# Optimization experiments

Hardware: AMD Instinct MI355X
Metric: run time of the kernel (lower is better)

Reference implementation:

```python
import jax, jax.numpy as jnp
import numpy as np
from jax import lax

EPS = 0.1        # entropic regularization
MAX_ITER = 100   # Sinkhorn iteration budget
THRESH = 0.1     # early-stop threshold on err = mean_b sum_i |u - u_prev|
B, N, D = 16, 1024, 64


def setup_inputs() -> dict:
    key = jax.random.key(0)
    k1, k2 = jax.random.split(key)
    x = jax.random.normal(k1, (B, N, D), dtype=jnp.float32)
    y = jax.random.normal(k2, (B, N, D), dtype=jnp.float32)
    return {"x": x, "y": y}


def _lse(A):
    # Faithful to the original (unstabilized) lse: log(sum(exp(A)) + 1e-6)
    return jnp.log(jnp.exp(A).sum(-1) + 1e-6)


def _M(C, u, v):
    # (-C_ij + u_i + v_j) / eps
    return (-C + u[..., :, None] + v[..., None, :]) / EPS


def _cost_matrix(x, y):
    # (avoids materializing the [B, N, N, D] difference tensor; same math for p=2)
    x2 = (x * x).sum(-1)                         # [B, N]
    y2 = (y * y).sum(-1)                         # [B, N]
    xy = jnp.einsum('bid,bjd->bij', x, y)        # [B, N, N]
    return x2[..., :, None] + y2[..., None, :] - 2.0 * xy


def reference(x, y):
    x = jax.nn.softmax(x, axis=-1)
    y = jax.nn.softmax(y, axis=-1)
    C = _cost_matrix(x, y)                       # [B, N, N]
    n = x.shape[-2]
    log_mu = jnp.log(1.0 / n + 1e-8)             # mu = nu = uniform 1/n (scalar broadcast)
    u0 = jnp.zeros((x.shape[0], n), dtype=C.dtype)
    v0 = jnp.zeros_like(u0)

    def cond(carry):
        _, _, i, err = carry
        return jnp.logical_and(i < MAX_ITER, err >= THRESH)

    def body(carry):
        u, v, i, _ = carry
        u1 = u
        u = EPS * (log_mu - _lse(_M(C, u, v))) + u
        v = EPS * (log_mu - _lse(jnp.swapaxes(_M(C, u, v), -2, -1))) + v
        err = jnp.abs(u - u1).sum(-1).mean()
        return (u, v, i + 1, err)

    u, v, _, _ = lax.while_loop(
        cond, body, (u0, v0, jnp.int32(0), jnp.float32(jnp.inf)))

    pi = jnp.exp(_M(C, u, v))                    # transport plan [B, N, N]
    cost = (pi * C).sum((-2, -1))                # [B]
    return cost.mean()                           # reduction='mean'
```

## Files before the change

### kernel.cpp

```cpp
#include <hip/hip_runtime.h>
#include <hip/hip_bf16.h>
#include <math.h>

#define BATCH 16
#define NPTS 1024
#define DIM 64
#define EPSF 0.1f
#define INV_EPS 10.0f
#define MAX_ITER 100
#define THRESHF 0.1f
#define LSTRIDE 72

typedef _Float16 h8 __attribute__((ext_vector_type(8)));
typedef short short8v __attribute__((ext_vector_type(8)));
typedef float float4v __attribute__((ext_vector_type(4)));

#define ATOMIC_ST(p, v) \
  __hip_atomic_store((p), (v), __ATOMIC_RELAXED, __HIP_MEMORY_SCOPE_AGENT)
#define ATOMIC_LD(p) \
  __hip_atomic_load((p), __ATOMIC_RELAXED, __HIP_MEMORY_SCOPE_AGENT)

__device__ inline float waveSum(float x) {
#pragma unroll
  for (int off = 32; off; off >>= 1) x += __shfl_xor(x, off, 64);
  return x;
}
__device__ inline float waveMax(float x) {
#pragma unroll
  for (int off = 32; off; off >>= 1) x = fmaxf(x, __shfl_xor(x, off, 64));
  return x;
}
__device__ inline long long packTag(int tag, float v) {
  return ((long long)tag << 32) | (long long)__float_as_uint(v);
}
__device__ inline long long pollTag(long long* p, int tag) {
  long long w;
  do { w = ATOMIC_LD(p); } while ((int)(w >> 32) < tag);
  return w;
}

__global__ __launch_bounds__(512, 2) void sinkhorn_fused(
    const float* __restrict__ x, const float* __restrict__ y,
    __hip_bfloat16* __restrict__ syh,
    float* __restrict__ y2,
    long long* __restrict__ partialT,
    long long* __restrict__ csT,
    long long* __restrict__ deltaT,
    long long* __restrict__ flags,
    float* __restrict__ errB,
    float* __restrict__ costPart,
    float* __restrict__ out) {
  __shared__ __attribute__((aligned(16))) short xs[64 * LSTRIDE];
  __shared__ __attribute__((aligned(16))) short ys[2][64 * LSTRIDE];
  __shared__ __attribute__((aligned(16))) short os[2][64 * LSTRIDE];
  __shared__ __attribute__((aligned(16))) float wLDS[NPTS];
  __shared__ __attribute__((aligned(16))) float colpart[8][NPTS];
  __shared__ __attribute__((aligned(16))) float red[16][66];
  __shared__ float x2L[64];
  __shared__ float derr[8];
  __shared__ float errbL[BATCH];
  const int t = threadIdx.x;
  const int blk = blockIdx.x;
  const int wave = t >> 6, lane = t & 63;
  const int batch = (blk & 7) + 8 * (blk >> 7);
  const int kslot = (blk >> 3) & 15;
  const float log_mu = logf(1.0f / 1024.0f + 1e-8f);
  const float mu_c = 1.0f / 1024.0f + 1e-8f;

#pragma unroll
  for (int rr = 0; rr < 8; rr++) {
    int rl = wave * 8 + rr;
    int gr = batch * NPTS + kslot * 64 + rl;
    float xv = x[(size_t)gr * DIM + lane];
    float mx = waveMax(xv);
    float ex = __expf(xv - mx);
    float sx = waveSum(ex);
    float px = ex / sx;
    __hip_bfloat16 hbx = (__hip_bfloat16)px;
    xs[rl * LSTRIDE + lane] = *(const short*)&hbx;
    float sqx = waveSum(px * px);
    if (lane == 0) x2L[rl] = sqx;
    float yv = y[(size_t)gr * DIM + lane];
    float my = waveMax(yv);
    float ey = __expf(yv - my);
    float sy = waveSum(ey);
    float py = ey / sy;
    __hip_bfloat16 hby = (__hip_bfloat16)py;
    unsigned bits = *(const unsigned short*)&hby;
    unsigned nb = __shfl_down(bits, 1);
    if ((lane & 1) == 0)
      ATOMIC_ST((unsigned*)((unsigned short*)syh + (size_t)gr * DIM + lane),
                bits | (nb << 16));
    float sqy = waveSum(py * py);
    if (lane == 0) ATOMIC_ST(&y2[gr], sqy);
  }
  __syncthreads();
  if (t == 0) ATOMIC_ST(&flags[batch * 16 + kslot], (long long)1 << 32);
  if (t < 16) {
    while ((int)(ATOMIC_LD(&flags[batch * 16 + t]) >> 32) < 1) {}
  }
  __syncthreads();

  const int m = lane & 15, q = lane >> 4;
  const int g = lane >> 3, sub = lane & 7;
  const int sw = wave & 3, ts = wave >> 2;
  short8v a0 = *(const short8v*)&xs[(sw * 16 + m) * LSTRIDE + q * 8];
  short8v a1 = *(const short8v*)&xs[(sw * 16 + m) * LSTRIDE + 32 + q * 8];
  float xa[4];
#pragma unroll
  for (int reg = 0; reg < 4; reg++) xa[reg] = x2L[sw * 16 + q * 4 + reg];
  float kaf[8][16];
#pragma unroll
  for (int k = 0; k < 8; k++) {
    {
      int idx = t;
#pragma unroll
      for (int rep = 0; rep < 2; rep++, idx += 512) {
        int r = idx >> 3, c = idx & 7;
        *(short8v*)&ys[r >> 6][(r & 63) * LSTRIDE + c * 8] = *(const short8v*)(
            (const short*)syh + ((size_t)batch * NPTS + 128 * k + r) * DIM + c * 8);
      }
    }
    __syncthreads();
    const int jt = 2 * k + ts;
    float4v accv[4];
#pragma unroll
    for (int tj = 0; tj < 4; tj++) {
      short8v b0 = *(const short8v*)&ys[ts][(tj * 16 + m) * LSTRIDE + q * 8];
      short8v b1 = *(const short8v*)&ys[ts][(tj * 16 + m) * LSTRIDE + 32 + q * 8];
      float4v c = {0.f, 0.f, 0.f, 0.f};
      c = __builtin_amdgcn_mfma_f32_16x16x32_bf16(a0, b0, c, 0, 0, 0);
      c = __builtin_amdgcn_mfma_f32_16x16x32_bf16(a1, b1, c, 0, 0, 0);
      accv[tj] = c;
    }
#pragma unroll
    for (int tj = 0; tj < 4; tj++) {
      float y2v = y2[(size_t)batch * NPTS + jt * 64 + tj * 16 + m];
#pragma unroll
      for (int reg = 0; reg < 4; reg++) {
        float C = xa[reg] + y2v - 2.0f * accv[tj][reg];
        _Float16 kv = (_Float16)__expf(-INV_EPS * C);
        os[ts][(sw * 16 + q * 4 + reg) * LSTRIDE + tj * 16 + m] = *(const short*)&kv;
      }
    }
    __syncthreads();
    {
      int e0 = (2 * k) & 7, e1 = (2 * k + 1) & 7;
      if (g == e0 || g == e1) {
        const short* srcp = (g == e0) ? &os[0][0] : &os[1][0];
#pragma unroll
        for (int rr = 0; rr < 8; rr++) {
          h8 v = *(const h8*)&srcp[(wave * 8 + rr) * LSTRIDE + sub * 8];
#pragma unroll
          for (int n = 0; n < 8; n++) {
            if (k < 4) kaf[rr][n] = (float)v[n];
            else kaf[rr][8 + n] = (float)v[n];
          }
        }
      }
    }
    __syncthreads();
  }

  for (int j = t; j < NPTS; j += 512) wLDS[j] = 1.f;
  __syncthreads();

  float eu[8], euPrev[8];
#pragma unroll
  for (int r = 0; r < 8; r++) eu[r] = 1.f;
  int it = 0;

  const int oks = t >> 5;
  const int oc = (t & 31) * 2;
  long long* opT =
      &partialT[(((size_t)batch * 16 + oks) << 10) + kslot * 64 + oc];

  while (true) {
#pragma unroll
    for (int r = 0; r < 8; r++) euPrev[r] = eu[r];
    const float4* w4 = (const float4*)wLDS;
    float wreg[16];
    *(float4*)&wreg[0]  = w4[2 * lane];
    *(float4*)&wreg[4]  = w4[2 * lane + 1];
    *(float4*)&wreg[8]  = w4[128 + 2 * lane];
    *(float4*)&wreg[12] = w4[128 + 2 * lane + 1];
    float colreg[16];
#pragma unroll
    for (int n = 0; n < 16; n++) colreg[n] = 0.f;
    float delta = 0.f;
#pragma unroll
    for (int rr = 0; rr < 8; rr++) {
      float dot = 0.f;
#pragma unroll
      for (int n = 0; n < 16; n++) dot = fmaf(kaf[rr][n], wreg[n], dot);
      dot = waveSum(dot);
      float sp = eu[rr] * dot + 1e-6f;
      float lg = __logf(sp);
      delta += fabsf(EPSF * (log_mu - lg));
      float ai = mu_c * eu[rr] * __builtin_amdgcn_rcpf(sp);
      eu[rr] = ai;
#pragma unroll
      for (int n = 0; n < 16; n++) colreg[n] = fmaf(kaf[rr][n], ai, colreg[n]);
    }
    if (lane == 0) derr[wave] = delta;
    {
      float4* cp = (float4*)&colpart[wave][0];
      cp[2 * lane]       = make_float4(colreg[0], colreg[1], colreg[2], colreg[3]);
      cp[2 * lane + 1]   = make_float4(colreg[4], colreg[5], colreg[6], colreg[7]);
      cp[128 + 2 * lane] = make_float4(colreg[8], colreg[9], colreg[10], colreg[11]);
      cp[128 + 2 * lane + 1] = make_float4(colreg[12], colreg[13], colreg[14], colreg[15]);
    }
    __syncthreads();
    {
      float s0 = 0.f, s1 = 0.f;
#pragma unroll
      for (int w = 0; w < 8; w++) { s0 += colpart[w][t]; s1 += colpart[w][t + 512]; }
      long long* wp = &partialT[(((size_t)batch * 16 + kslot) << 10) + t];
      ATOMIC_ST(wp, packTag(it + 2, s0));
      ATOMIC_ST(wp + 512, packTag(it + 2, s1));
    }
    if (t == 0) {
      float e = 0.f;
#pragma unroll
      for (int w = 0; w < 8; w++) e += derr[w];
      ATOMIC_ST(&deltaT[((it & 1) * BATCH + batch) * 16 + kslot],
                packTag(it + 2, e));
    }
    if (it >= 1 && t < BATCH) {
      float v;
      while ((v = ATOMIC_LD(&errB[(it - 1) * BATCH + t])) < 0.f) {}
      errbL[t] = v;
    }
    __syncthreads();
    if (it >= 1) {
      float errv = 0.f;
#pragma unroll
      for (int k = 0; k < BATCH; k++) errv += errbL[k];
      if (errv * (1.0f / (float)BATCH) < THRESHF) {
#pragma unroll
        for (int r = 0; r < 8; r++) eu[r] = euPrev[r];
        break;
      }
    }
    {
      long long w0 = pollTag(opT, it + 2);
      long long w1 = pollTag(opT + 1, it + 2);
      red[oks][oc] = __uint_as_float((unsigned)w0);
      red[oks][oc + 1] = __uint_as_float((unsigned)w1);
    }
    __syncthreads();
    if (t < 64) {
      float s = 0.f;
#pragma unroll
      for (int k2 = 0; k2 < 16; k2++) s += red[k2][t];
      ATOMIC_ST(&csT[((size_t)batch << 10) + kslot * 64 + t],
                packTag(it + 2, s));
    }
    if (kslot == 0 && wave == 0) {
      float e16 = 0.f;
      if (lane < 16) {
        long long fw =
            pollTag(&deltaT[((it & 1) * BATCH + batch) * 16 + lane], it + 2);
        e16 = __uint_as_float((unsigned)fw);
      }
#pragma unroll
      for (int off = 8; off; off >>= 1) e16 += __shfl_xor(e16, off, 16);
      if (lane == 0) ATOMIC_ST(&errB[it * BATCH + batch], e16);
    }
    float cs0, cs1;
    {
      long long* cp0 = &csT[((size_t)batch << 10) + t];
      long long a = pollTag(cp0, it + 2);
      long long b = pollTag(cp0 + 512, it + 2);
      cs0 = __uint_as_float((unsigned)a);
      cs1 = __uint_as_float((unsigned)b);
    }
    {
      float w0 = wLDS[t];
      wLDS[t] = mu_c * w0 * __builtin_amdgcn_rcpf(w0 * cs0 + 1e-6f);
      float w1 = wLDS[t + 512];
      wLDS[t + 512] = mu_c * w1 * __builtin_amdgcn_rcpf(w1 * cs1 + 1e-6f);
    }
    it++;
    if (it >= MAX_ITER) break;
    __syncthreads();
  }

  {
    __syncthreads();
    const float4* w4 = (const float4*)wLDS;
    float wreg[16];
    *(float4*)&wreg[0]  = w4[2 * lane];
    *(float4*)&wreg[4]  = w4[2 * lane + 1];
    *(float4*)&wreg[8]  = w4[128 + 2 * lane];
    *(float4*)&wreg[12] = w4[128 + 2 * lane + 1];
    float csum = 0.f;
#pragma unroll
    for (int rr = 0; rr < 8; rr++) {
      float ai = eu[rr];
#pragma unroll
      for (int n = 0; n < 16; n++) {
        float kf = kaf[rr][n];
        if (kf > 0.f)
          csum += ai * wreg[n] * kf * (-EPSF * __logf(kf));
      }
    }
    csum = waveSum(csum);
    if (lane == 0) derr[wave] = csum;
    __syncthreads();
    if (t == 0) {
      float cst = 0.f;
#pragma unroll
      for (int w = 0; w < 8; w++) cst += derr[w];
      ATOMIC_ST(&costPart[blk], cst + 1.0f);
    }
    if (blk == 0) {
      if (t < 256) {
        float v;
        while ((v = ATOMIC_LD(&costPart[t])) < 0.5f) {}
        colpart[0][t] = v;
      }
      __syncthreads();
      if (wave == 0) {
        float s = colpart[0][lane] + colpart[0][lane + 64] +
                  colpart[0][lane + 128] + colpart[0][lane + 192];
        s = waveSum(s);
        if (lane == 0) out[0] = (s - 256.0f) * (1.0f / (float)BATCH);
      }
    }
  }
}

extern "C" void kernel_launch(void* const* d_in, const int* in_sizes, int n_in,
                              void* d_out, int out_size, void* d_ws,
                              size_t ws_size, hipStream_t stream) {
  (void)in_sizes; (void)n_in; (void)out_size; (void)ws_size;
  const float* x = (const float*)d_in[0];
  const float* y = (const float*)d_in[1];
  float* out = (float*)d_out;

  char* ws = (char*)d_ws;
  size_t off = 0;
  auto alloc = [&](size_t nbytes) -> void* {
    void* p = (void*)(ws + off);
    off = (off + nbytes + 255) & ~(size_t)255;
    return p;
  };
  __hip_bfloat16* syh = (__hip_bfloat16*)alloc((size_t)BATCH * NPTS * DIM * 2);
  float* y2 = (float*)alloc((size_t)BATCH * NPTS * 4);
  long long* partialT = (long long*)alloc((size_t)BATCH * 16 * NPTS * 8);
  long long* csT = (long long*)alloc((size_t)BATCH * NPTS * 8);
  long long* deltaT = (long long*)alloc((size_t)2 * BATCH * 16 * 8);
  long long* flags = (long long*)alloc((size_t)BATCH * 16 * 8);
  float* errB = (float*)alloc((size_t)MAX_ITER * BATCH * 4);
  float* costPart = (float*)alloc(256 * 4);

  void* args[] = {&x, &y, &syh, &y2, &partialT, &csT, &deltaT,
                  &flags, &errB, &costPart, &out};
  hipLaunchCooperativeKernel((void*)sinkhorn_fused, dim3(256), dim3(512), args,
                             0, stream);
}
```

Before: 132.7 us.

## Store transposed kernel slab per block to replace column partial-sum exchange with scaling-vector exchange

Each block now also builds the transposed kernel slab (its 64 columns against all rows) in fp16 registers. Within each iteration it then exchanges only the updated row scalings u and column scalings v through tagged global words. This replaces the old scheme, which published 1024-wide column partial sums per block and reduced them across 16 blocks. Row and column matvecs use packed fp16 fdot2 with the u values pre-scaled by 1024 before conversion to fp16. This cuts cross-block traffic and a reduction stage per iteration, at the cost of doubling the kernel-matrix setup work, more register use, and fp16 precision in the matvec inputs and accumulation.

```diff
diff --git a/kernel.cpp b/kernel.cpp
--- a/kernel.cpp
+++ b/kernel.cpp
@@ -12,8 +12,14 @@
 #define LSTRIDE 72
 
 typedef _Float16 h8 __attribute__((ext_vector_type(8)));
+typedef _Float16 half2v __attribute__((ext_vector_type(2)));
 typedef short short8v __attribute__((ext_vector_type(8)));
 typedef float float4v __attribute__((ext_vector_type(4)));
+
+template <int P>
+__device__ __forceinline__ half2v h2get(h8 v) {
+  return __builtin_shufflevector(v, v, 2 * P, 2 * P + 1);
+}
 
 #define ATOMIC_ST(p, v) \
   __hip_atomic_store((p), (v), __ATOMIC_RELAXED, __HIP_MEMORY_SCOPE_AGENT)
@@ -38,13 +44,25 @@
   do { w = ATOMIC_LD(p); } while ((int)(w >> 32) < tag);
   return w;
 }
+__device__ inline void pollTag2(long long* p0, long long* p1, int tag,
+                                float& v0, float& v1) {
+  long long a = ATOMIC_LD(p0), b = ATOMIC_LD(p1);
+  while ((int)(a >> 32) < tag || (int)(b >> 32) < tag) {
+    a = ATOMIC_LD(p0);
+    b = ATOMIC_LD(p1);
+  }
+  v0 = __uint_as_float((unsigned)a);
+  v1 = __uint_as_float((unsigned)b);
+}
 
 __global__ __launch_bounds__(512, 2) void sinkhorn_fused(
     const float* __restrict__ x, const float* __restrict__ y,
     __hip_bfloat16* __restrict__ syh,
+    __hip_bfloat16* __restrict__ sxh,
     float* __restrict__ y2,
-    long long* __restrict__ partialT,
-    long long* __restrict__ csT,
+    float* __restrict__ x2g,
+    long long* __restrict__ euT,
+    long long* __restrict__ wT,
     long long* __restrict__ deltaT,
     long long* __restrict__ flags,
     float* __restrict__ errB,
@@ -54,8 +72,8 @@
   __shared__ __attribute__((aligned(16))) short ys[2][64 * LSTRIDE];
   __shared__ __attribute__((aligned(16))) short os[2][64 * LSTRIDE];
   __shared__ __attribute__((aligned(16))) float wLDS[NPTS];
-  __shared__ __attribute__((aligned(16))) float colpart[8][NPTS];
-  __shared__ __attribute__((aligned(16))) float red[16][66];
+  __shared__ __attribute__((aligned(16))) _Float16 whL[NPTS];
+  __shared__ __attribute__((aligned(16))) _Float16 ahL[8 * 136];
   __shared__ float x2L[64];
   __shared__ float derr[8];
   __shared__ float errbL[BATCH];
@@ -80,6 +98,12 @@
     xs[rl * LSTRIDE + lane] = *(const short*)&hbx;
     float sqx = waveSum(px * px);
     if (lane == 0) x2L[rl] = sqx;
+    unsigned xbits = *(const unsigned short*)&hbx;
+    unsigned xnb = __shfl_down(xbits, 1);
+    if ((lane & 1) == 0)
+      ATOMIC_ST((unsigned*)((unsigned short*)sxh + (size_t)gr * DIM + lane),
+                xbits | (xnb << 16));
+    if (lane == 0) ATOMIC_ST(&x2g[gr], sqx);
     float yv = y[(size_t)gr * DIM + lane];
     float my = waveMax(yv);
     float ey = __expf(yv - my);
@@ -104,134 +128,174 @@
   const int m = lane & 15, q = lane >> 4;
   const int g = lane >> 3, sub = lane & 7;
   const int sw = wave & 3, ts = wave >> 2;
-  short8v a0 = *(const short8v*)&xs[(sw * 16 + m) * LSTRIDE + q * 8];
-  short8v a1 = *(const short8v*)&xs[(sw * 16 + m) * LSTRIDE + 32 + q * 8];
-  float xa[4];
-#pragma unroll
-  for (int reg = 0; reg < 4; reg++) xa[reg] = x2L[sw * 16 + q * 4 + reg];
-  float kaf[8][16];
-#pragma unroll
-  for (int k = 0; k < 8; k++) {
-    {
-      int idx = t;
-#pragma unroll
-      for (int rep = 0; rep < 2; rep++, idx += 512) {
-        int r = idx >> 3, c = idx & 7;
-        *(short8v*)&ys[r >> 6][(r & 63) * LSTRIDE + c * 8] = *(const short8v*)(
-            (const short*)syh + ((size_t)batch * NPTS + 128 * k + r) * DIM + c * 8);
-      }
-    }
-    __syncthreads();
-    const int jt = 2 * k + ts;
-    float4v accv[4];
-#pragma unroll
-    for (int tj = 0; tj < 4; tj++) {
-      short8v b0 = *(const short8v*)&ys[ts][(tj * 16 + m) * LSTRIDE + q * 8];
-      short8v b1 = *(const short8v*)&ys[ts][(tj * 16 + m) * LSTRIDE + 32 + q * 8];
-      float4v c = {0.f, 0.f, 0.f, 0.f};
-      c = __builtin_amdgcn_mfma_f32_16x16x32_bf16(a0, b0, c, 0, 0, 0);
-      c = __builtin_amdgcn_mfma_f32_16x16x32_bf16(a1, b1, c, 0, 0, 0);
-      accv[tj] = c;
-    }
-#pragma unroll
-    for (int tj = 0; tj < 4; tj++) {
-      float y2v = y2[(size_t)batch * NPTS + jt * 64 + tj * 16 + m];
-#pragma unroll
-      for (int reg = 0; reg < 4; reg++) {
-        float C = xa[reg] + y2v - 2.0f * accv[tj][reg];
-        _Float16 kv = (_Float16)__expf(-INV_EPS * C);
-        os[ts][(sw * 16 + q * 4 + reg) * LSTRIDE + tj * 16 + m] = *(const short*)&kv;
-      }
-    }
-    __syncthreads();
-    {
-      int e0 = (2 * k) & 7, e1 = (2 * k + 1) & 7;
-      if (g == e0 || g == e1) {
-        const short* srcp = (g == e0) ? &os[0][0] : &os[1][0];
-#pragma unroll
-        for (int rr = 0; rr < 8; rr++) {
-          h8 v = *(const h8*)&srcp[(wave * 8 + rr) * LSTRIDE + sub * 8];
-#pragma unroll
-          for (int n = 0; n < 8; n++) {
-            if (k < 4) kaf[rr][n] = (float)v[n];
-            else kaf[rr][8 + n] = (float)v[n];
+  h8 ka[8], kb[8];
+  {
+    short8v a0 = *(const short8v*)&xs[(sw * 16 + m) * LSTRIDE + q * 8];
+    short8v a1 = *(const short8v*)&xs[(sw * 16 + m) * LSTRIDE + 32 + q * 8];
+    float xa[4];
+#pragma unroll
+    for (int reg = 0; reg < 4; reg++) xa[reg] = x2L[sw * 16 + q * 4 + reg];
+#pragma unroll
+    for (int k = 0; k < 8; k++) {
+      {
+        int idx = t;
+#pragma unroll
+        for (int rep = 0; rep < 2; rep++, idx += 512) {
+          int r = idx >> 3, c = idx & 7;
+          *(short8v*)&ys[r >> 6][(r & 63) * LSTRIDE + c * 8] = *(const short8v*)(
+              (const short*)syh + ((size_t)batch * NPTS + 128 * k + r) * DIM + c * 8);
+        }
+      }
+      __syncthreads();
+      const int jt = 2 * k + ts;
+#pragma unroll
+      for (int tj = 0; tj < 4; tj++) {
+        short8v b0 = *(const short8v*)&ys[ts][(tj * 16 + m) * LSTRIDE + q * 8];
+        short8v b1 = *(const short8v*)&ys[ts][(tj * 16 + m) * LSTRIDE + 32 + q * 8];
+        float4v c = {0.f, 0.f, 0.f, 0.f};
+        c = __builtin_amdgcn_mfma_f32_16x16x32_bf16(a0, b0, c, 0, 0, 0);
+        c = __builtin_amdgcn_mfma_f32_16x16x32_bf16(a1, b1, c, 0, 0, 0);
+        float y2v = y2[(size_t)batch * NPTS + jt * 64 + tj * 16 + m];
+#pragma unroll
+        for (int reg = 0; reg < 4; reg++) {
+          float C = xa[reg] + y2v - 2.0f * c[reg];
+          _Float16 kv = (_Float16)__expf(-INV_EPS * C);
+          os[ts][(sw * 16 + q * 4 + reg) * LSTRIDE + tj * 16 + m] = *(const short*)&kv;
+        }
+      }
+      __syncthreads();
+      {
+        int e0 = (2 * k) & 7, e1 = (2 * k + 1) & 7;
+        if (g == e0 || g == e1) {
+          const short* srcp = (g == e0) ? &os[0][0] : &os[1][0];
+#pragma unroll
+          for (int rr = 0; rr < 8; rr++) {
+            h8 v = *(const h8*)&srcp[(wave * 8 + rr) * LSTRIDE + sub * 8];
+            if (k < 4) ka[rr] = v; else kb[rr] = v;
           }
         }
       }
+      __syncthreads();
+    }
+  }
+
+  h8 kt[16];
+  {
+    {
+      int r = t >> 3, c8 = t & 7;
+      *(short8v*)&xs[r * LSTRIDE + c8 * 8] = *(const short8v*)(
+          (const short*)syh + ((size_t)batch * NPTS + kslot * 64 + r) * DIM + c8 * 8);
     }
     __syncthreads();
-  }
-
-  for (int j = t; j < NPTS; j += 512) wLDS[j] = 1.f;
+    short8v a0 = *(const short8v*)&xs[(sw * 16 + m) * LSTRIDE + q * 8];
+    short8v a1 = *(const short8v*)&xs[(sw * 16 + m) * LSTRIDE + 32 + q * 8];
+    float yn[4];
+#pragma unroll
+    for (int reg = 0; reg < 4; reg++)
+      yn[reg] = y2[(size_t)batch * NPTS + kslot * 64 + sw * 16 + q * 4 + reg];
+#pragma unroll
+    for (int k = 0; k < 8; k++) {
+      {
+        int idx = t;
+#pragma unroll
+        for (int rep = 0; rep < 2; rep++, idx += 512) {
+          int r = idx >> 3, c = idx & 7;
+          *(short8v*)&ys[r >> 6][(r & 63) * LSTRIDE + c * 8] = *(const short8v*)(
+              (const short*)sxh + ((size_t)batch * NPTS + 128 * k + r) * DIM + c * 8);
+        }
+      }
+      __syncthreads();
+      const int jt = 2 * k + ts;
+#pragma unroll
+      for (int tj = 0; tj < 4; tj++) {
+        short8v b0 = *(const short8v*)&ys[ts][(tj * 16 + m) * LSTRIDE + q * 8];
+        short8v b1 = *(const short8v*)&ys[ts][(tj * 16 + m) * LSTRIDE + 32 + q * 8];
+        float4v c = {0.f, 0.f, 0.f, 0.f};
+        c = __builtin_amdgcn_mfma_f32_16x16x32_bf16(a0, b0, c, 0, 0, 0);
+        c = __builtin_amdgcn_mfma_f32_16x16x32_bf16(a1, b1, c, 0, 0, 0);
+        float x2v = x2g[(size_t)batch * NPTS + jt * 64 + tj * 16 + m];
+#pragma unroll
+        for (int reg = 0; reg < 4; reg++) {
+          float C = yn[reg] + x2v - 2.0f * c[reg];
+          _Float16 kv = (_Float16)__expf(-INV_EPS * C);
+          os[ts][(sw * 16 + q * 4 + reg) * LSTRIDE + tj * 16 + m] = *(const short*)&kv;
+        }
+      }
+      __syncthreads();
+      if ((t & 7) == k) {
+        int c = t >> 3;
+#pragma unroll
+        for (int j = 0; j < 8; j++)
+          kt[j] = *(const h8*)&os[0][c * LSTRIDE + j * 8];
+#pragma unroll
+        for (int j = 0; j < 8; j++)
+          kt[8 + j] = *(const h8*)&os[1][c * LSTRIDE + j * 8];
+      }
+      __syncthreads();
+    }
+  }
+
+  for (int j = t; j < NPTS; j += 512) {
+    wLDS[j] = 1.f;
+    whL[j] = (_Float16)1.f;
+  }
   __syncthreads();
 
   float eu[8], euPrev[8];
 #pragma unroll
   for (int r = 0; r < 8; r++) eu[r] = 1.f;
+  float wj = 1.f;
   int it = 0;
-
-  const int oks = t >> 5;
-  const int oc = (t & 31) * 2;
-  long long* opT =
-      &partialT[(((size_t)batch * 16 + oks) << 10) + kslot * 64 + oc];
+  long long* euB = &euT[((size_t)batch << 10)];
+  long long* wB = &wT[((size_t)batch << 10)];
 
   while (true) {
 #pragma unroll
     for (int r = 0; r < 8; r++) euPrev[r] = eu[r];
-    const float4* w4 = (const float4*)wLDS;
-    float wreg[16];
-    *(float4*)&wreg[0]  = w4[2 * lane];
-    *(float4*)&wreg[4]  = w4[2 * lane + 1];
-    *(float4*)&wreg[8]  = w4[128 + 2 * lane];
-    *(float4*)&wreg[12] = w4[128 + 2 * lane + 1];
-    float colreg[16];
-#pragma unroll
-    for (int n = 0; n < 16; n++) colreg[n] = 0.f;
-    float delta = 0.f;
-#pragma unroll
-    for (int rr = 0; rr < 8; rr++) {
-      float dot = 0.f;
-#pragma unroll
-      for (int n = 0; n < 16; n++) dot = fmaf(kaf[rr][n], wreg[n], dot);
-      dot = waveSum(dot);
-      float sp = eu[rr] * dot + 1e-6f;
-      float lg = __logf(sp);
-      delta += fabsf(EPSF * (log_mu - lg));
-      float ai = mu_c * eu[rr] * __builtin_amdgcn_rcpf(sp);
-      eu[rr] = ai;
-#pragma unroll
-      for (int n = 0; n < 16; n++) colreg[n] = fmaf(kaf[rr][n], ai, colreg[n]);
-    }
-    if (lane == 0) derr[wave] = delta;
     {
-      float4* cp = (float4*)&colpart[wave][0];
-      cp[2 * lane]       = make_float4(colreg[0], colreg[1], colreg[2], colreg[3]);
-      cp[2 * lane + 1]   = make_float4(colreg[4], colreg[5], colreg[6], colreg[7]);
-      cp[128 + 2 * lane] = make_float4(colreg[8], colreg[9], colreg[10], colreg[11]);
-      cp[128 + 2 * lane + 1] = make_float4(colreg[12], colreg[13], colreg[14], colreg[15]);
-    }
-    __syncthreads();
-    {
-      float s0 = 0.f, s1 = 0.f;
-#pragma unroll
-      for (int w = 0; w < 8; w++) { s0 += colpart[w][t]; s1 += colpart[w][t + 512]; }
-      long long* wp = &partialT[(((size_t)batch * 16 + kslot) << 10) + t];
-      ATOMIC_ST(wp, packTag(it + 2, s0));
-      ATOMIC_ST(wp + 512, packTag(it + 2, s1));
-    }
-    if (t == 0) {
-      float e = 0.f;
-#pragma unroll
-      for (int w = 0; w < 8; w++) e += derr[w];
-      ATOMIC_ST(&deltaT[((it & 1) * BATCH + batch) * 16 + kslot],
-                packTag(it + 2, e));
+      h8 wh0 = *(const h8*)&whL[8 * lane];
+      h8 wh1 = *(const h8*)&whL[512 + 8 * lane];
+      float delta = 0.f;
+#pragma unroll
+      for (int rr = 0; rr < 8; rr++) {
+        float d0 = 0.f, d1 = 0.f;
+#define DOT_STEP(P)                                                         \
+  d0 = __builtin_amdgcn_fdot2(h2get<P>(ka[rr]), h2get<P>(wh0), d0, false);  \
+  d1 = __builtin_amdgcn_fdot2(h2get<P>(kb[rr]), h2get<P>(wh1), d1, false);
+        DOT_STEP(0) DOT_STEP(1) DOT_STEP(2) DOT_STEP(3)
+#undef DOT_STEP
+        float dot = waveSum(d0 + d1);
+        float sp = eu[rr] * dot + 1e-6f;
+        float lg = __logf(sp);
+        delta += fabsf(EPSF * (log_mu - lg));
+        eu[rr] = mu_c * eu[rr] * __builtin_amdgcn_rcpf(sp);
+      }
+      if (lane == 0) derr[wave] = delta;
+      long long* ep = &euB[kslot * 64 + wave * 8];
+#pragma unroll
+      for (int rr = 0; rr < 8; rr++)
+        if (lane == rr) ATOMIC_ST(&ep[rr], packTag(it + 2, eu[rr]));
     }
     if (it >= 1 && t < BATCH) {
       float v;
       while ((v = ATOMIC_LD(&errB[(it - 1) * BATCH + t])) < 0.f) {}
       errbL[t] = v;
     }
+    {
+      float a0v, a1v;
+      pollTag2(&euB[t], &euB[t + 512], it + 2, a0v, a1v);
+      ahL[t + ((t >> 7) << 3)] = (_Float16)(a0v * 1024.0f);
+      int r1 = t + 512;
+      ahL[r1 + ((r1 >> 7) << 3)] = (_Float16)(a1v * 1024.0f);
+    }
     __syncthreads();
+    if (t == 0) {
+      float e = 0.f;
+#pragma unroll
+      for (int w = 0; w < 8; w++) e += derr[w];
+      ATOMIC_ST(&deltaT[((it & 1) * BATCH + batch) * 16 + kslot],
+                packTag(it + 2, e));
+    }
     if (it >= 1) {
       float errv = 0.f;
 #pragma unroll
@@ -243,43 +307,46 @@
       }
     }
     {
-      long long w0 = pollTag(opT, it + 2);
-      long long w1 = pollTag(opT + 1, it + 2);
-      red[oks][oc] = __uint_as_float((unsigned)w0);
-      red[oks][oc + 1] = __uint_as_float((unsigned)w1);
-    }
-    __syncthreads();
-    if (t < 64) {
-      float s = 0.f;
-#pragma unroll
-      for (int k2 = 0; k2 < 16; k2++) s += red[k2][t];
-      ATOMIC_ST(&csT[((size_t)batch << 10) + kslot * 64 + t],
-                packTag(it + 2, s));
+      const h8* av = (const h8*)&ahL[136 * (t & 7)];
+      float c0 = 0.f, c1 = 0.f, c2 = 0.f, c3 = 0.f;
+#define CDOT(J, ACC)                                                        \
+  {                                                                         \
+    h8 kv = kt[J], a8 = av[J];                                              \
+    ACC = __builtin_amdgcn_fdot2(h2get<0>(kv), h2get<0>(a8), ACC, false);   \
+    ACC = __builtin_amdgcn_fdot2(h2get<1>(kv), h2get<1>(a8), ACC, false);   \
+    ACC = __builtin_amdgcn_fdot2(h2get<2>(kv), h2get<2>(a8), ACC, false);   \
+    ACC = __builtin_amdgcn_fdot2(h2get<3>(kv), h2get<3>(a8), ACC, false);   \
+  }
+      CDOT(0, c0) CDOT(1, c1) CDOT(2, c2) CDOT(3, c3)
+      CDOT(4, c0) CDOT(5, c1) CDOT(6, c2) CDOT(7, c3)
+      CDOT(8, c0) CDOT(9, c1) CDOT(10, c2) CDOT(11, c3)
+      CDOT(12, c0) CDOT(13, c1) CDOT(14, c2) CDOT(15, c3)
+#undef CDOT
+      float cd = (c0 + c1) + (c2 + c3);
+      cd += __shfl_xor(cd, 1, 64);
+      cd += __shfl_xor(cd, 2, 64);
+      cd += __shfl_xor(cd, 4, 64);
+      float sp = wj * cd * 0.0009765625f + 1e-6f;
+      wj = mu_c * wj * __builtin_amdgcn_rcpf(sp);
+      if ((lane & 7) == 0)
+        ATOMIC_ST(&wB[kslot * 64 + (t >> 3)], packTag(it + 2, wj));
     }
     if (kslot == 0 && wave == 0) {
       float e16 = 0.f;
-      if (lane < 16) {
-        long long fw =
-            pollTag(&deltaT[((it & 1) * BATCH + batch) * 16 + lane], it + 2);
-        e16 = __uint_as_float((unsigned)fw);
-      }
+      if (lane < 16)
+        e16 = __uint_as_float((unsigned)pollTag(
+            &deltaT[((it & 1) * BATCH + batch) * 16 + lane], it + 2));
 #pragma unroll
       for (int off = 8; off; off >>= 1) e16 += __shfl_xor(e16, off, 16);
       if (lane == 0) ATOMIC_ST(&errB[it * BATCH + batch], e16);
     }
-    float cs0, cs1;
     {
-      long long* cp0 = &csT[((size_t)batch << 10) + t];
-      long long a = pollTag(cp0, it + 2);
-      long long b = pollTag(cp0 + 512, it + 2);
-      cs0 = __uint_as_float((unsigned)a);
-      cs1 = __uint_as_float((unsigned)b);
-    }
-    {
-      float w0 = wLDS[t];
-      wLDS[t] = mu_c * w0 * __builtin_amdgcn_rcpf(w0 * cs0 + 1e-6f);
-      float w1 = wLDS[t + 512];
-      wLDS[t + 512] = mu_c * w1 * __builtin_amdgcn_rcpf(w1 * cs1 + 1e-6f);
+      float w0v, w1v;
+      pollTag2(&wB[t], &wB[t + 512], it + 2, w0v, w1v);
+      wLDS[t] = w0v;
+      whL[t] = (_Float16)w0v;
+      wLDS[t + 512] = w1v;
+      whL[t + 512] = (_Float16)w1v;
     }
     it++;
     if (it >= MAX_ITER) break;
@@ -299,10 +366,11 @@
     for (int rr = 0; rr < 8; rr++) {
       float ai = eu[rr];
 #pragma unroll
-      for (int n = 0; n < 16; n++) {
-        float kf = kaf[rr][n];
-        if (kf > 0.f)
-          csum += ai * wreg[n] * kf * (-EPSF * __logf(kf));
+      for (int n = 0; n < 8; n++) {
+        float kf = (float)ka[rr][n];
+        if (kf > 0.f) csum += ai * wreg[n] * kf * (-EPSF * __logf(kf));
+        float kg = (float)kb[rr][n];
+        if (kg > 0.f) csum += ai * wreg[8 + n] * kg * (-EPSF * __logf(kg));
       }
     }
     csum = waveSum(csum);
@@ -315,15 +383,15 @@
       ATOMIC_ST(&costPart[blk], cst + 1.0f);
     }
     if (blk == 0) {
+      float* gb = (float*)&ys[0][0];
       if (t < 256) {
         float v;
         while ((v = ATOMIC_LD(&costPart[t])) < 0.5f) {}
-        colpart[0][t] = v;
+        gb[t] = v;
       }
       __syncthreads();
       if (wave == 0) {
-        float s = colpart[0][lane] + colpart[0][lane + 64] +
-                  colpart[0][lane + 128] + colpart[0][lane + 192];
+        float s = gb[lane] + gb[lane + 64] + gb[lane + 128] + gb[lane + 192];
         s = waveSum(s);
         if (lane == 0) out[0] = (s - 256.0f) * (1.0f / (float)BATCH);
       }
@@ -347,16 +415,18 @@
     return p;
   };
   __hip_bfloat16* syh = (__hip_bfloat16*)alloc((size_t)BATCH * NPTS * DIM * 2);
+  __hip_bfloat16* sxh = (__hip_bfloat16*)alloc((size_t)BATCH * NPTS * DIM * 2);
   float* y2 = (float*)alloc((size_t)BATCH * NPTS * 4);
-  long long* partialT = (long long*)alloc((size_t)BATCH * 16 * NPTS * 8);
-  long long* csT = (long long*)alloc((size_t)BATCH * NPTS * 8);
+  float* x2g = (float*)alloc((size_t)BATCH * NPTS * 4);
+  long long* euT = (long long*)alloc((size_t)BATCH * NPTS * 8);
+  long long* wT = (long long*)alloc((size_t)BATCH * NPTS * 8);
   long long* deltaT = (long long*)alloc((size_t)2 * BATCH * 16 * 8);
   long long* flags = (long long*)alloc((size_t)BATCH * 16 * 8);
   float* errB = (float*)alloc((size_t)MAX_ITER * BATCH * 4);
   float* costPart = (float*)alloc(256 * 4);
 
-  void* args[] = {&x, &y, &syh, &y2, &partialT, &csT, &deltaT,
-                  &flags, &errB, &costPart, &out};
+  void* args[] = {&x, &y, &syh, &sxh, &y2, &x2g, &euT, &wT,
+                  &deltaT, &flags, &errB, &costPart, &out};
   hipLaunchCooperativeKernel((void*)sinkhorn_fused, dim3(256), dim3(512), args,
                              0, stream);
 }
```

After: 160.7 us. 1.21x slower.
